# Optimization experiments

Hardware: AMD Instinct MI355X
Metric: run time of the kernel (lower is better)

## Reference

```python
import jax, jax.numpy as jnp
import numpy as np

HEADS = 16
DIM_HEAD = 64
RMS_EPS = 1.1920929e-07  # torch.finfo(float32).eps (torch RMSNorm eps=None default)
ROPE_THETA = 10000.0


def _rope(x):
    # x: [b, h, n, d]; rotary-embedding-torch style interleaved rotation
    n, d = x.shape[-2], x.shape[-1]
    inv_freq = 1.0 / (ROPE_THETA ** (jnp.arange(0, d, 2, dtype=jnp.float32) / d))
    t = jnp.arange(n, dtype=jnp.float32)
    freqs = t[:, None] * inv_freq[None, :]              # [n, d/2]
    cos = jnp.repeat(jnp.cos(freqs), 2, axis=-1)        # [n, d] interleaved
    sin = jnp.repeat(jnp.sin(freqs), 2, axis=-1)
    x1 = x[..., ::2]
    x2 = x[..., 1::2]
    rot = jnp.stack((-x2, x1), axis=-1).reshape(x.shape)  # rotate_half, interleaved pairs
    return x * cos + rot * sin


def setup_inputs() -> dict:
    key = jax.random.key(0)
    ks = jax.random.split(key, 6)
    b, n, dim = 2, 2048, 1024
    tokens = jax.random.normal(ks[0], (b, n, dim), dtype=jnp.float32)
    norm_weight = jnp.ones((dim,), dtype=jnp.float32)
    wq = jax.random.normal(ks[1], (dim, dim), dtype=jnp.float32) * 0.02
    wk = jax.random.normal(ks[2], (dim, dim), dtype=jnp.float32) * 0.02
    wv = jax.random.normal(ks[3], (dim, dim), dtype=jnp.float32) * 0.02
    wo = jax.random.normal(ks[4], (dim, dim), dtype=jnp.float32) * 0.02
    return {"tokens": tokens, "norm_weight": norm_weight, "wq": wq, "wk": wk, "wv": wv, "wo": wo}


def reference(tokens, norm_weight, wq, wk, wv, wo):
    b, n, dim = tokens.shape
    # RMSNorm (elementwise affine)
    x = tokens * jax.lax.rsqrt(jnp.mean(tokens * tokens, axis=-1, keepdims=True) + RMS_EPS)
    x = x * norm_weight
    # QKV projections (torch Linear: x @ W.T), split heads: b n (h d) -> b h n d
    def split(y):
        return y.reshape(b, n, HEADS, DIM_HEAD).transpose(0, 2, 1, 3)
    q = split(x @ wq.T) * (DIM_HEAD ** -0.5)
    k = split(x @ wk.T)
    v = split(x @ wv.T)
    # rotary embedding (no kv cache -> same positions for q and k)
    q = _rope(q)
    k = _rope(k)
    sim = jnp.einsum('bhid,bhjd->bhij', q, k)
    causal = jnp.triu(jnp.ones((n, n), dtype=bool), k=1)
    sim = jnp.where(causal, -jnp.finfo(sim.dtype).max, sim)
    attn = jax.nn.softmax(sim, axis=-1)
    out = jnp.einsum('bhij,bhjd->bhid', attn, v)
    out = out.transpose(0, 2, 1, 3).reshape(b, n, dim)  # merge heads
    return out @ wo.T
```

## Files before the change

kernel.cpp:

```cpp
#include <hip/hip_runtime.h>

typedef __bf16 bf16x8 __attribute__((ext_vector_type(8)));
typedef float f32x4 __attribute__((ext_vector_type(4)));

#define DIM 1024
#define NSEQ 2048

#define GL2LDS(g, l) __builtin_amdgcn_global_load_lds( \
    (const __attribute__((address_space(1))) void*)(g), \
    (__attribute__((address_space(3))) void*)(l), 16, 0, 0)

__global__ __launch_bounds__(256) void cvt_kernel(const float* __restrict__ s,
                                                  __bf16* __restrict__ d) {
    int i = (blockIdx.x * 256 + threadIdx.x) * 4;
    float4 f = *(const float4*)(s + i);
    union { uint2 u; __bf16 h[4]; } p;
    p.h[0] = (__bf16)f.x; p.h[1] = (__bf16)f.y;
    p.h[2] = (__bf16)f.z; p.h[3] = (__bf16)f.w;
    *(uint2*)(d + i) = p.u;
}

__global__ __launch_bounds__(256) void cvt3_kernel(const float* __restrict__ wq,
                                                   const float* __restrict__ wk,
                                                   const float* __restrict__ wv,
                                                   __bf16* __restrict__ dq,
                                                   __bf16* __restrict__ dk,
                                                   __bf16* __restrict__ dv,
                                                   int* __restrict__ counters) {
    if (blockIdx.x == 0 && blockIdx.y == 0 && threadIdx.x < 8)
        counters[threadIdx.x] = 0;
    const float* s = blockIdx.y == 0 ? wq : (blockIdx.y == 1 ? wk : wv);
    __bf16*      d = blockIdx.y == 0 ? dq : (blockIdx.y == 1 ? dk : dv);
    int i = (blockIdx.x * 256 + threadIdx.x) * 4;
    float4 f = *(const float4*)(s + i);
    union { uint2 u; __bf16 h[4]; } p;
    p.h[0] = (__bf16)f.x; p.h[1] = (__bf16)f.y;
    p.h[2] = (__bf16)f.z; p.h[3] = (__bf16)f.w;
    *(uint2*)(d + i) = p.u;
}

__global__ __launch_bounds__(256) void rmsnorm_kernel(const float* __restrict__ x,
                                                      const float* __restrict__ g,
                                                      __bf16* __restrict__ o) {
    int row = blockIdx.x;
    int t = threadIdx.x;
    float4 xv = ((const float4*)(x + (size_t)row * DIM))[t];
    float ss = xv.x*xv.x + xv.y*xv.y + xv.z*xv.z + xv.w*xv.w;
    #pragma unroll
    for (int off = 32; off; off >>= 1) ss += __shfl_xor(ss, off, 64);
    __shared__ float red[4];
    if ((t & 63) == 0) red[t >> 6] = ss;
    __syncthreads();
    ss = red[0] + red[1] + red[2] + red[3];
    float r = rsqrtf(ss * (1.0f / 1024.0f) + 1.1920929e-07f);
    float4 gv = ((const float4*)g)[t];
    union { uint2 u; __bf16 h[4]; } p;
    p.h[0] = (__bf16)(xv.x * r * gv.x);
    p.h[1] = (__bf16)(xv.y * r * gv.y);
    p.h[2] = (__bf16)(xv.z * r * gv.z);
    p.h[3] = (__bf16)(xv.w * r * gv.w);
    *(uint2*)(o + (size_t)row * DIM + t * 4) = p.u;
}

__global__ __launch_bounds__(256) void rope_kernel(__bf16* __restrict__ qb,
                                                   __bf16* __restrict__ kb) {
    int bid = blockIdx.x;
    __bf16* x = (bid & 1) ? kb : qb;
    int gid = (bid >> 1) * 256 + threadIdx.x;
    int row = gid >> 9;
    int pr = gid & 511;
    int pos = row & (NSEQ - 1);
    int dp = pr & 31;
    float inv = __expf(-(float)dp * (9.210340371976184f / 32.0f));
    float ang = (float)pos * inv;
    float sn, cs;
    sincosf(ang, &sn, &cs);
    size_t off = (size_t)row * DIM + pr * 2;
    union { unsigned int u; __bf16 h[2]; } p;
    p.u = *(const unsigned int*)(x + off);
    float x1 = (float)p.h[0], x2 = (float)p.h[1];
    p.h[0] = (__bf16)(x1 * cs - x2 * sn);
    p.h[1] = (__bf16)(x2 * cs + x1 * sn);
    *(unsigned int*)(x + off) = p.u;
}

template <typename CT>
__device__ __forceinline__ void gemm_body(const __bf16* __restrict__ A,
                                          const __bf16* __restrict__ B,
                                          CT* __restrict__ C,
                                          int mb, int nb, int ldc, float scale,
                                          __bf16* As, __bf16* Bs) {
    int t = threadIdx.x;
    int w = t >> 6, l = t & 63;
    int wm = (w >> 1) * 64, wn = (w & 1) * 64;
    int lrow = l & 15, lq = l >> 4;
    f32x4 acc[4][4] = {};

    int srow = w * 32 + (l >> 3);
    int sc8 = (l & 7) * 8;
    const __bf16* gA = A + (size_t)(mb * 128 + srow) * 1024 + sc8;
    const __bf16* gB = B + (size_t)(nb * 128 + srow) * 1024 + sc8;
    __bf16* lA = As + (size_t)(w * 32) * 64;
    __bf16* lB = Bs + (size_t)(w * 32) * 64;

    for (int kt = 0; kt < 16; ++kt) {
        int k0 = kt * 64;
        #pragma unroll
        for (int c = 0; c < 4; ++c) {
            GL2LDS(gA + (size_t)c * 8 * 1024 + k0, lA + c * 8 * 64);
            GL2LDS(gB + (size_t)c * 8 * 1024 + k0, lB + c * 8 * 64);
        }
        __syncthreads();
        #pragma unroll
        for (int ch = 0; ch < 2; ++ch) {
            bf16x8 af[4], bfr[4];
            #pragma unroll
            for (int i = 0; i < 4; ++i)
                af[i] = *(const bf16x8*)&As[(wm + i * 16 + lrow) * 64 + ch * 32 + lq * 8];
            #pragma unroll
            for (int i = 0; i < 4; ++i)
                bfr[i] = *(const bf16x8*)&Bs[(wn + i * 16 + lrow) * 64 + ch * 32 + lq * 8];
            #pragma unroll
            for (int rt = 0; rt < 4; ++rt)
                #pragma unroll
                for (int ct = 0; ct < 4; ++ct)
                    acc[rt][ct] = __builtin_amdgcn_mfma_f32_16x16x32_bf16(
                        af[rt], bfr[ct], acc[rt][ct], 0, 0, 0);
        }
        __syncthreads();
    }
    #pragma unroll
    for (int rt = 0; rt < 4; ++rt)
        #pragma unroll
        for (int ct = 0; ct < 4; ++ct)
            #pragma unroll
            for (int r = 0; r < 4; ++r) {
                int row = mb * 128 + wm + rt * 16 + lq * 4 + r;
                int col = nb * 128 + wn + ct * 16 + lrow;
                C[(size_t)row * ldc + col] = (CT)(acc[rt][ct][r] * scale);
            }
}

__global__ __launch_bounds__(256) void qkv_kernel(const __bf16* __restrict__ x,
                                                  const __bf16* __restrict__ wq,
                                                  const __bf16* __restrict__ wk,
                                                  const __bf16* __restrict__ wv,
                                                  __bf16* __restrict__ qb,
                                                  __bf16* __restrict__ kb,
                                                  __bf16* __restrict__ vtb) {
    __shared__ __bf16 As[128 * 64];
    __shared__ __bf16 Bs[128 * 64];
    int bm = blockIdx.x, bn = blockIdx.y, z = blockIdx.z;
    if (z == 0)      gemm_body<__bf16>(x,  wq, qb,  bm, bn, 1024,
                                       0.125f * 1.44269504088896340736f, As, Bs);
    else if (z == 1) gemm_body<__bf16>(x,  wk, kb,  bm, bn, 1024, 1.0f,   As, Bs);
    else             gemm_body<__bf16>(wv, x,  vtb, bn, bm, 4096, 1.0f,   As, Bs);
}

__global__ __launch_bounds__(256) void wo_kernel(const __bf16* __restrict__ A,
                                                 const __bf16* __restrict__ B,
                                                 float* __restrict__ C) {
    __shared__ __bf16 As[128 * 64];
    __shared__ __bf16 Bs[128 * 64];
    gemm_body<float>(A, B, C, blockIdx.x, blockIdx.y, 1024, 1.0f, As, Bs);
}

__global__ __launch_bounds__(256, 3) void attn_kernel(const __bf16* __restrict__ q,
                                                      const __bf16* __restrict__ kk,
                                                      const __bf16* __restrict__ vt,
                                                      __bf16* __restrict__ o,
                                                      int* __restrict__ counters) {
    int xcd = blockIdx.x & 7;
    int t = threadIdx.x;
    int w = t >> 6, l = t & 63;
    int lrow = l & 15, lq = l >> 4;
    int row0 = t >> 3;
    int c8 = (t & 7) * 8;

    __shared__ __bf16 Kt[2][64 * 72];
    __shared__ __bf16 Vs[2][64 * 72];
    __shared__ __bf16 Ps[4 * 16 * 72];
    __shared__ int s_item;
    __bf16* pw = &Ps[w * 16 * 72];

    for (;;) {
        if (t == 0) s_item = atomicAdd(&counters[xcd], 1);
        __syncthreads();
        int item = s_item;
        if (item >= 128) break;
        int qt = 31 - (item >> 2);
        int bh = xcd * 4 + (item & 3);
        int h = bh & 15;
        int b = bh >> 4;
        int rowbase = b * NSEQ;

        const __bf16* kbase = kk + (size_t)rowbase * DIM + h * 64;
        const __bf16* vbase = vt + (size_t)(h * 64) * 4096 + b * 2048;

        const __bf16* qp = q + (size_t)(rowbase + qt * 64 + w * 16 + lrow) * DIM + h * 64;
        bf16x8 qb0 = *(const bf16x8*)(qp + lq * 8);
        bf16x8 qb1 = *(const bf16x8*)(qp + 32 + lq * 8);

        f32x4 oacc[4] = {};
        float m_r = -1e30f, l_r = 0.0f;

        uint4 kr0, kr1, vr0, vr1;
        kr0 = *(const uint4*)(kbase + (size_t)row0 * DIM + c8);
        kr1 = *(const uint4*)(kbase + (size_t)(row0 + 32) * DIM + c8);
        vr0 = *(const uint4*)(vbase + (size_t)row0 * 4096 + c8);
        vr1 = *(const uint4*)(vbase + (size_t)(row0 + 32) * 4096 + c8);
        *(uint4*)&Kt[0][row0 * 72 + c8] = kr0;
        *(uint4*)&Kt[0][(row0 + 32) * 72 + c8] = kr1;
        *(uint4*)&Vs[0][row0 * 72 + c8] = vr0;
        *(uint4*)&Vs[0][(row0 + 32) * 72 + c8] = vr1;
        __syncthreads();

        for (int jt = 0; jt <= qt; ++jt) {
            int cur = jt & 1;
            if (jt < qt) {
                int j0 = (jt + 1) * 64;
                kr0 = *(const uint4*)(kbase + (size_t)(j0 + row0) * DIM + c8);
                kr1 = *(const uint4*)(kbase + (size_t)(j0 + row0 + 32) * DIM + c8);
                vr0 = *(const uint4*)(vbase + (size_t)row0 * 4096 + j0 + c8);
                vr1 = *(const uint4*)(vbase + (size_t)(row0 + 32) * 4096 + j0 + c8);
            }
            f32x4 st[4];
            #pragma unroll
            for (int ct = 0; ct < 4; ++ct) {
                f32x4 z = {};
                bf16x8 ka0 = *(const bf16x8*)&Kt[cur][(ct * 16 + lrow) * 72 + lq * 8];
                bf16x8 ka1 = *(const bf16x8*)&Kt[cur][(ct * 16 + lrow) * 72 + 32 + lq * 8];
                z = __builtin_amdgcn_mfma_f32_16x16x32_bf16(ka0, qb0, z, 0, 0, 0);
                z = __builtin_amdgcn_mfma_f32_16x16x32_bf16(ka1, qb1, z, 0, 0, 0);
                st[ct] = z;
            }
            if (jt == qt) {
                int qr = w * 16 + lrow;
                #pragma unroll
                for (int ct = 0; ct < 4; ++ct)
                    #pragma unroll
                    for (int r = 0; r < 4; ++r)
                        if (ct * 16 + lq * 4 + r > qr) st[ct][r] = -3.0e38f;
            }
            float mx = st[0][0];
            #pragma unroll
            for (int ct = 0; ct < 4; ++ct)
                #pragma unroll
                for (int r = 0; r < 4; ++r) mx = fmaxf(mx, st[ct][r]);
            mx = fmaxf(mx, __shfl_xor(mx, 16, 64));
            mx = fmaxf(mx, __shfl_xor(mx, 32, 64));
            if (!__all(mx - m_r <= 8.0f)) {
                float mnew = fmaxf(m_r, mx);
                float alpha = __builtin_amdgcn_exp2f(m_r - mnew);
                l_r *= alpha;
                #pragma unroll
                for (int ct = 0; ct < 4; ++ct)
                    #pragma unroll
                    for (int r = 0; r < 4; ++r) oacc[ct][r] *= alpha;
                m_r = mnew;
            }
            float ps = 0.0f;
            #pragma unroll
            for (int ct = 0; ct < 4; ++ct)
                #pragma unroll
                for (int r = 0; r < 4; ++r) {
                    float p = __builtin_amdgcn_exp2f(st[ct][r] - m_r);
                    st[ct][r] = p;
                    ps += p;
                }
            ps += __shfl_xor(ps, 16, 64);
            ps += __shfl_xor(ps, 32, 64);
            l_r += ps;

            #pragma unroll
            for (int ct = 0; ct < 4; ++ct) {
                union { uint2 u; __bf16 h4[4]; } pk;
                #pragma unroll
                for (int r = 0; r < 4; ++r) pk.h4[r] = (__bf16)st[ct][r];
                *(uint2*)&pw[lrow * 72 + ct * 16 + lq * 4] = pk.u;
            }
            bf16x8 pb0 = *(const bf16x8*)&pw[lrow * 72 + lq * 8];
            bf16x8 pb1 = *(const bf16x8*)&pw[lrow * 72 + 32 + lq * 8];
            #pragma unroll
            for (int ct = 0; ct < 4; ++ct) {
                bf16x8 va0 = *(const bf16x8*)&Vs[cur][(ct * 16 + lrow) * 72 + lq * 8];
                bf16x8 va1 = *(const bf16x8*)&Vs[cur][(ct * 16 + lrow) * 72 + 32 + lq * 8];
                oacc[ct] = __builtin_amdgcn_mfma_f32_16x16x32_bf16(va0, pb0, oacc[ct], 0, 0, 0);
                oacc[ct] = __builtin_amdgcn_mfma_f32_16x16x32_bf16(va1, pb1, oacc[ct], 0, 0, 0);
            }
            if (jt < qt) {
                *(uint4*)&Kt[cur ^ 1][row0 * 72 + c8] = kr0;
                *(uint4*)&Kt[cur ^ 1][(row0 + 32) * 72 + c8] = kr1;
                *(uint4*)&Vs[cur ^ 1][row0 * 72 + c8] = vr0;
                *(uint4*)&Vs[cur ^ 1][(row0 + 32) * 72 + c8] = vr1;
            }
            __syncthreads();
        }
        float rcp = 1.0f / l_r;
        const size_t orow = (size_t)(rowbase + qt * 64 + w * 16 + lrow) * DIM + h * 64;
        #pragma unroll
        for (int ct = 0; ct < 4; ++ct) {
            union { uint2 u; __bf16 h4[4]; } pk;
            #pragma unroll
            for (int r = 0; r < 4; ++r) pk.h4[r] = (__bf16)(oacc[ct][r] * rcp);
            *(uint2*)(o + orow + ct * 16 + lq * 4) = pk.u;
        }
    }
}

extern "C" void kernel_launch(void* const* d_in, const int* in_sizes, int n_in,
                              void* d_out, int out_size, void* d_ws, size_t ws_size,
                              hipStream_t stream) {
    const float* tokens = (const float*)d_in[0];
    const float* gamma  = (const float*)d_in[1];
    const float* wq = (const float*)d_in[2];
    const float* wk = (const float*)d_in[3];
    const float* wv = (const float*)d_in[4];
    const float* wo = (const float*)d_in[5];

    __bf16* ws  = (__bf16*)d_ws;
    __bf16* x   = ws;
    __bf16* qb  = x   + (size_t)4096 * 1024;
    __bf16* kb  = qb  + (size_t)4096 * 1024;
    __bf16* vtb = kb  + (size_t)4096 * 1024;
    __bf16* ao  = x;
    __bf16* wob = qb;
    float*  out = (float*)d_out;

    __bf16* wqb = (__bf16*)d_out;
    __bf16* wkb = wqb + (size_t)1024 * 1024;
    __bf16* wvb = wkb + (size_t)1024 * 1024;
    int* counters = (int*)((char*)d_out + (size_t)8 * 1024 * 1024);

    cvt3_kernel<<<dim3(1024, 3), 256, 0, stream>>>(wq, wk, wv, wqb, wkb, wvb, counters);

    rmsnorm_kernel<<<4096, 256, 0, stream>>>(tokens, gamma, x);

    qkv_kernel<<<dim3(32, 8, 3), 256, 0, stream>>>(x, wqb, wkb, wvb, qb, kb, vtb);

    rope_kernel<<<16384, 256, 0, stream>>>(qb, kb);

    attn_kernel<<<768, 256, 0, stream>>>(qb, kb, vtb, ao, counters);

    cvt_kernel<<<1024, 256, 0, stream>>>(wo, wob);

    wo_kernel<<<dim3(32, 8), 256, 0, stream>>>(ao, wob, out);
}
```

Measured before the change: 206.2 us.

## Software-pipeline QK^T one tile ahead of softmax in causal flash attention

Restructures the attention inner loop so the QK^T MFMAs for the next key tile are issued before the softmax of the current tile. Scores ping-pong between two register sets, global prefetch runs two tiles ahead, and s_setprio raises wave priority around the MFMA blocks. The max and sum reductions are also rewritten as trees to shorten dependency chains. In exchange it uses more registers, which may lower occupancy, and adds an extra barrier per iteration around the LDS buffer writes.

```diff
diff --git a/kernel.cpp b/kernel.cpp
--- a/kernel.cpp
+++ b/kernel.cpp
@@ -203,8 +203,9 @@
 
         f32x4 oacc[4] = {};
         float m_r = -1e30f, l_r = 0.0f;
-
+        f32x4 stA[4], stB[4];
         uint4 kr0, kr1, vr0, vr1;
+
         kr0 = *(const uint4*)(kbase + (size_t)row0 * DIM + c8);
         kr1 = *(const uint4*)(kbase + (size_t)(row0 + 32) * DIM + c8);
         vr0 = *(const uint4*)(vbase + (size_t)row0 * 4096 + c8);
@@ -213,26 +214,55 @@
         *(uint4*)&Kt[0][(row0 + 32) * 72 + c8] = kr1;
         *(uint4*)&Vs[0][row0 * 72 + c8] = vr0;
         *(uint4*)&Vs[0][(row0 + 32) * 72 + c8] = vr1;
+        if (qt >= 1) {
+            kr0 = *(const uint4*)(kbase + (size_t)(64 + row0) * DIM + c8);
+            kr1 = *(const uint4*)(kbase + (size_t)(64 + row0 + 32) * DIM + c8);
+            vr0 = *(const uint4*)(vbase + (size_t)row0 * 4096 + 64 + c8);
+            vr1 = *(const uint4*)(vbase + (size_t)(row0 + 32) * 4096 + 64 + c8);
+        }
         __syncthreads();
-
-        for (int jt = 0; jt <= qt; ++jt) {
-            int cur = jt & 1;
-            if (jt < qt) {
-                int j0 = (jt + 1) * 64;
+        __builtin_amdgcn_s_setprio(1);
+        #pragma unroll
+        for (int ct = 0; ct < 4; ++ct) {
+            f32x4 z = {};
+            bf16x8 ka0 = *(const bf16x8*)&Kt[0][(ct * 16 + lrow) * 72 + lq * 8];
+            bf16x8 ka1 = *(const bf16x8*)&Kt[0][(ct * 16 + lrow) * 72 + 32 + lq * 8];
+            z = __builtin_amdgcn_mfma_f32_16x16x32_bf16(ka0, qb0, z, 0, 0, 0);
+            z = __builtin_amdgcn_mfma_f32_16x16x32_bf16(ka1, qb1, z, 0, 0, 0);
+            stA[ct] = z;
+        }
+        __builtin_amdgcn_s_setprio(0);
+        if (qt >= 1) {
+            *(uint4*)&Kt[1][row0 * 72 + c8] = kr0;
+            *(uint4*)&Kt[1][(row0 + 32) * 72 + c8] = kr1;
+            *(uint4*)&Vs[1][row0 * 72 + c8] = vr0;
+            *(uint4*)&Vs[1][(row0 + 32) * 72 + c8] = vr1;
+            __syncthreads();
+        }
+
+        auto trip = [&](f32x4 (&sc)[4], f32x4 (&sn)[4], int jt) {
+            bool nx1 = jt + 1 <= qt;
+            bool nx2 = jt + 2 <= qt;
+            if (nx2) {
+                int j0 = (jt + 2) * 64;
                 kr0 = *(const uint4*)(kbase + (size_t)(j0 + row0) * DIM + c8);
                 kr1 = *(const uint4*)(kbase + (size_t)(j0 + row0 + 32) * DIM + c8);
                 vr0 = *(const uint4*)(vbase + (size_t)row0 * 4096 + j0 + c8);
                 vr1 = *(const uint4*)(vbase + (size_t)(row0 + 32) * 4096 + j0 + c8);
             }
-            f32x4 st[4];
-            #pragma unroll
-            for (int ct = 0; ct < 4; ++ct) {
-                f32x4 z = {};
-                bf16x8 ka0 = *(const bf16x8*)&Kt[cur][(ct * 16 + lrow) * 72 + lq * 8];
-                bf16x8 ka1 = *(const bf16x8*)&Kt[cur][(ct * 16 + lrow) * 72 + 32 + lq * 8];
-                z = __builtin_amdgcn_mfma_f32_16x16x32_bf16(ka0, qb0, z, 0, 0, 0);
-                z = __builtin_amdgcn_mfma_f32_16x16x32_bf16(ka1, qb1, z, 0, 0, 0);
-                st[ct] = z;
+            if (nx1) {
+                int kc = (jt + 1) & 1;
+                __builtin_amdgcn_s_setprio(1);
+                #pragma unroll
+                for (int ct = 0; ct < 4; ++ct) {
+                    f32x4 z = {};
+                    bf16x8 ka0 = *(const bf16x8*)&Kt[kc][(ct * 16 + lrow) * 72 + lq * 8];
+                    bf16x8 ka1 = *(const bf16x8*)&Kt[kc][(ct * 16 + lrow) * 72 + 32 + lq * 8];
+                    z = __builtin_amdgcn_mfma_f32_16x16x32_bf16(ka0, qb0, z, 0, 0, 0);
+                    z = __builtin_amdgcn_mfma_f32_16x16x32_bf16(ka1, qb1, z, 0, 0, 0);
+                    sn[ct] = z;
+                }
+                __builtin_amdgcn_s_setprio(0);
             }
             if (jt == qt) {
                 int qr = w * 16 + lrow;
@@ -240,13 +270,13 @@
                 for (int ct = 0; ct < 4; ++ct)
                     #pragma unroll
                     for (int r = 0; r < 4; ++r)
-                        if (ct * 16 + lq * 4 + r > qr) st[ct][r] = -3.0e38f;
-            }
-            float mx = st[0][0];
-            #pragma unroll
-            for (int ct = 0; ct < 4; ++ct)
-                #pragma unroll
-                for (int r = 0; r < 4; ++r) mx = fmaxf(mx, st[ct][r]);
+                        if (ct * 16 + lq * 4 + r > qr) sc[ct][r] = -3.0e38f;
+            }
+            float m0 = fmaxf(fmaxf(sc[0][0], sc[0][1]), fmaxf(sc[0][2], sc[0][3]));
+            float m1 = fmaxf(fmaxf(sc[1][0], sc[1][1]), fmaxf(sc[1][2], sc[1][3]));
+            float m2 = fmaxf(fmaxf(sc[2][0], sc[2][1]), fmaxf(sc[2][2], sc[2][3]));
+            float m3 = fmaxf(fmaxf(sc[3][0], sc[3][1]), fmaxf(sc[3][2], sc[3][3]));
+            float mx = fmaxf(fmaxf(m0, m1), fmaxf(m2, m3));
             mx = fmaxf(mx, __shfl_xor(mx, 16, 64));
             mx = fmaxf(mx, __shfl_xor(mx, 32, 64));
             if (!__all(mx - m_r <= 8.0f)) {
@@ -259,15 +289,19 @@
                     for (int r = 0; r < 4; ++r) oacc[ct][r] *= alpha;
                 m_r = mnew;
             }
-            float ps = 0.0f;
-            #pragma unroll
-            for (int ct = 0; ct < 4; ++ct)
+            float psum[4];
+            #pragma unroll
+            for (int ct = 0; ct < 4; ++ct) {
+                float s = 0.0f;
                 #pragma unroll
                 for (int r = 0; r < 4; ++r) {
-                    float p = __builtin_amdgcn_exp2f(st[ct][r] - m_r);
-                    st[ct][r] = p;
-                    ps += p;
+                    float p = __builtin_amdgcn_exp2f(sc[ct][r] - m_r);
+                    sc[ct][r] = p;
+                    s += p;
                 }
+                psum[ct] = s;
+            }
+            float ps = (psum[0] + psum[1]) + (psum[2] + psum[3]);
             ps += __shfl_xor(ps, 16, 64);
             ps += __shfl_xor(ps, 32, 64);
             l_r += ps;
@@ -276,26 +310,42 @@
             for (int ct = 0; ct < 4; ++ct) {
                 union { uint2 u; __bf16 h4[4]; } pk;
                 #pragma unroll
-                for (int r = 0; r < 4; ++r) pk.h4[r] = (__bf16)st[ct][r];
+                for (int r = 0; r < 4; ++r) pk.h4[r] = (__bf16)sc[ct][r];
                 *(uint2*)&pw[lrow * 72 + ct * 16 + lq * 4] = pk.u;
             }
             bf16x8 pb0 = *(const bf16x8*)&pw[lrow * 72 + lq * 8];
             bf16x8 pb1 = *(const bf16x8*)&pw[lrow * 72 + 32 + lq * 8];
+            int vc = jt & 1;
+            __builtin_amdgcn_s_setprio(1);
             #pragma unroll
             for (int ct = 0; ct < 4; ++ct) {
-                bf16x8 va0 = *(const bf16x8*)&Vs[cur][(ct * 16 + lrow) * 72 + lq * 8];
-                bf16x8 va1 = *(const bf16x8*)&Vs[cur][(ct * 16 + lrow) * 72 + 32 + lq * 8];
+                bf16x8 va0 = *(const bf16x8*)&Vs[vc][(ct * 16 + lrow) * 72 + lq * 8];
+                bf16x8 va1 = *(const bf16x8*)&Vs[vc][(ct * 16 + lrow) * 72 + 32 + lq * 8];
                 oacc[ct] = __builtin_amdgcn_mfma_f32_16x16x32_bf16(va0, pb0, oacc[ct], 0, 0, 0);
                 oacc[ct] = __builtin_amdgcn_mfma_f32_16x16x32_bf16(va1, pb1, oacc[ct], 0, 0, 0);
             }
-            if (jt < qt) {
-                *(uint4*)&Kt[cur ^ 1][row0 * 72 + c8] = kr0;
-                *(uint4*)&Kt[cur ^ 1][(row0 + 32) * 72 + c8] = kr1;
-                *(uint4*)&Vs[cur ^ 1][row0 * 72 + c8] = vr0;
-                *(uint4*)&Vs[cur ^ 1][(row0 + 32) * 72 + c8] = vr1;
-            }
-            __syncthreads();
-        }
+            __builtin_amdgcn_s_setprio(0);
+            if (nx2) {
+                __syncthreads();
+                int sb = jt & 1;
+                *(uint4*)&Kt[sb][row0 * 72 + c8] = kr0;
+                *(uint4*)&Kt[sb][(row0 + 32) * 72 + c8] = kr1;
+                *(uint4*)&Vs[sb][row0 * 72 + c8] = vr0;
+                *(uint4*)&Vs[sb][(row0 + 32) * 72 + c8] = vr1;
+                __syncthreads();
+            }
+        };
+
+        int jt = 0;
+        for (;;) {
+            trip(stA, stB, jt);
+            if (jt == qt) break;
+            ++jt;
+            trip(stB, stA, jt);
+            if (jt == qt) break;
+            ++jt;
+        }
+
         float rcp = 1.0f / l_r;
         const size_t orow = (size_t)(rowbase + qt * 64 + w * 16 + lrow) * DIM + h * 64;
         #pragma unroll
```

After: 204.4 us. About the same (-0.8%).

## Make attention waves independent with register-resident K/V and per-wave work stealing

Applied to the files above, without the earlier changes.

The attention kernel no longer stages K and V tiles through shared memory with block-wide barriers. Each wave now claims its own 32-row query tile from the per-XCD atomic counter and loads K/V fragments straight from global memory into registers, double-buffered through a two-step unrolled loop. The grid shrinks to 256 blocks and the occupancy hint is dropped. This removes the __syncthreads and LDS round-trips and improves causal load balance. In exchange, each wave re-reads K/V from L2 separately, which raises global traffic, and register pressure goes up.

```diff
diff --git a/kernel.cpp b/kernel.cpp
--- a/kernel.cpp
+++ b/kernel.cpp
@@ -9,6 +9,8 @@
 #define GL2LDS(g, l) __builtin_amdgcn_global_load_lds( \
     (const __attribute__((address_space(1))) void*)(g), \
     (__attribute__((address_space(3))) void*)(l), 16, 0, 0)
+
+#define MFMA16(a, b, c) __builtin_amdgcn_mfma_f32_16x16x32_bf16(a, b, c, 0, 0, 0)
 
 __global__ __launch_bounds__(256) void cvt_kernel(const float* __restrict__ s,
                                                   __bf16* __restrict__ d) {
@@ -124,8 +126,7 @@
             for (int rt = 0; rt < 4; ++rt)
                 #pragma unroll
                 for (int ct = 0; ct < 4; ++ct)
-                    acc[rt][ct] = __builtin_amdgcn_mfma_f32_16x16x32_bf16(
-                        af[rt], bfr[ct], acc[rt][ct], 0, 0, 0);
+                    acc[rt][ct] = MFMA16(af[rt], bfr[ct], acc[rt][ct]);
         }
         __syncthreads();
     }
@@ -165,145 +166,169 @@
     gemm_body<float>(A, B, C, blockIdx.x, blockIdx.y, 1024, 1.0f, As, Bs);
 }
 
-__global__ __launch_bounds__(256, 3) void attn_kernel(const __bf16* __restrict__ q,
-                                                      const __bf16* __restrict__ kk,
-                                                      const __bf16* __restrict__ vt,
-                                                      __bf16* __restrict__ o,
-                                                      int* __restrict__ counters) {
+__global__ __launch_bounds__(256) void attn_kernel(const __bf16* __restrict__ q,
+                                                   const __bf16* __restrict__ kk,
+                                                   const __bf16* __restrict__ vt,
+                                                   __bf16* __restrict__ o,
+                                                   int* __restrict__ counters) {
     int xcd = blockIdx.x & 7;
     int t = threadIdx.x;
     int w = t >> 6, l = t & 63;
     int lrow = l & 15, lq = l >> 4;
-    int row0 = t >> 3;
-    int c8 = (t & 7) * 8;
-
-    __shared__ __bf16 Kt[2][64 * 72];
-    __shared__ __bf16 Vs[2][64 * 72];
-    __shared__ __bf16 Ps[4 * 16 * 72];
-    __shared__ int s_item;
-    __bf16* pw = &Ps[w * 16 * 72];
+
+    __shared__ __bf16 Ps[4][32 * 76];
+    __bf16* pw = Ps[w];
 
     for (;;) {
-        if (t == 0) s_item = atomicAdd(&counters[xcd], 1);
-        __syncthreads();
-        int item = s_item;
-        if (item >= 128) break;
-        int qt = 31 - (item >> 2);
-        int bh = xcd * 4 + (item & 3);
+        int it = 0;
+        if (l == 0) it = atomicAdd(&counters[xcd], 1);
+        it = __shfl(it, 0, 64);
+        if (it >= 256) break;
+        int qq = 63 - (it >> 2);
+        int bh = xcd * 4 + (it & 3);
         int h = bh & 15;
         int b = bh >> 4;
         int rowbase = b * NSEQ;
+        int JT = qq >> 1;
 
         const __bf16* kbase = kk + (size_t)rowbase * DIM + h * 64;
         const __bf16* vbase = vt + (size_t)(h * 64) * 4096 + b * 2048;
 
-        const __bf16* qp = q + (size_t)(rowbase + qt * 64 + w * 16 + lrow) * DIM + h * 64;
-        bf16x8 qb0 = *(const bf16x8*)(qp + lq * 8);
-        bf16x8 qb1 = *(const bf16x8*)(qp + 32 + lq * 8);
-
-        f32x4 oacc[4] = {};
-        float m_r = -1e30f, l_r = 0.0f;
-
-        uint4 kr0, kr1, vr0, vr1;
-        kr0 = *(const uint4*)(kbase + (size_t)row0 * DIM + c8);
-        kr1 = *(const uint4*)(kbase + (size_t)(row0 + 32) * DIM + c8);
-        vr0 = *(const uint4*)(vbase + (size_t)row0 * 4096 + c8);
-        vr1 = *(const uint4*)(vbase + (size_t)(row0 + 32) * 4096 + c8);
-        *(uint4*)&Kt[0][row0 * 72 + c8] = kr0;
-        *(uint4*)&Kt[0][(row0 + 32) * 72 + c8] = kr1;
-        *(uint4*)&Vs[0][row0 * 72 + c8] = vr0;
-        *(uint4*)&Vs[0][(row0 + 32) * 72 + c8] = vr1;
-        __syncthreads();
-
-        for (int jt = 0; jt <= qt; ++jt) {
-            int cur = jt & 1;
-            if (jt < qt) {
-                int j0 = (jt + 1) * 64;
-                kr0 = *(const uint4*)(kbase + (size_t)(j0 + row0) * DIM + c8);
-                kr1 = *(const uint4*)(kbase + (size_t)(j0 + row0 + 32) * DIM + c8);
-                vr0 = *(const uint4*)(vbase + (size_t)row0 * 4096 + j0 + c8);
-                vr1 = *(const uint4*)(vbase + (size_t)(row0 + 32) * 4096 + j0 + c8);
-            }
-            f32x4 st[4];
-            #pragma unroll
-            for (int ct = 0; ct < 4; ++ct) {
-                f32x4 z = {};
-                bf16x8 ka0 = *(const bf16x8*)&Kt[cur][(ct * 16 + lrow) * 72 + lq * 8];
-                bf16x8 ka1 = *(const bf16x8*)&Kt[cur][(ct * 16 + lrow) * 72 + 32 + lq * 8];
-                z = __builtin_amdgcn_mfma_f32_16x16x32_bf16(ka0, qb0, z, 0, 0, 0);
-                z = __builtin_amdgcn_mfma_f32_16x16x32_bf16(ka1, qb1, z, 0, 0, 0);
-                st[ct] = z;
-            }
-            if (jt == qt) {
-                int qr = w * 16 + lrow;
+        bf16x8 qf[2][2];
+        #pragma unroll
+        for (int g = 0; g < 2; ++g) {
+            const __bf16* qp = q + (size_t)(rowbase + qq * 32 + g * 16 + lrow) * DIM + h * 64;
+            qf[g][0] = *(const bf16x8*)(qp + lq * 8);
+            qf[g][1] = *(const bf16x8*)(qp + 32 + lq * 8);
+        }
+
+        f32x4 oacc[2][4] = {};
+        float m_r[2] = {-1e30f, -1e30f};
+        float l_r[2] = {0.0f, 0.0f};
+
+        bf16x8 kA[8], kB[8], vA[8], vB[8];
+        #pragma unroll
+        for (int ct = 0; ct < 4; ++ct) {
+            const __bf16* kp = kbase + (size_t)(ct * 16 + lrow) * DIM;
+            kA[ct * 2]     = *(const bf16x8*)(kp + lq * 8);
+            kA[ct * 2 + 1] = *(const bf16x8*)(kp + 32 + lq * 8);
+            const __bf16* vp = vbase + (size_t)(ct * 16 + lrow) * 4096;
+            vA[ct * 2]     = *(const bf16x8*)(vp + lq * 8);
+            vA[ct * 2 + 1] = *(const bf16x8*)(vp + 32 + lq * 8);
+        }
+
+        auto trip = [&](bf16x8 (&kc)[8], bf16x8 (&kn)[8],
+                        bf16x8 (&vc)[8], bf16x8 (&vn)[8], int jt) {
+            f32x4 st[2][4];
+            #pragma unroll
+            for (int ct = 0; ct < 4; ++ct)
+                #pragma unroll
+                for (int g = 0; g < 2; ++g) {
+                    f32x4 z = {};
+                    z = MFMA16(kc[ct * 2],     qf[g][0], z);
+                    z = MFMA16(kc[ct * 2 + 1], qf[g][1], z);
+                    st[g][ct] = z;
+                }
+            if (jt < JT) {
+                int j1 = (jt + 1) * 64;
+                #pragma unroll
+                for (int ct = 0; ct < 4; ++ct) {
+                    const __bf16* kp = kbase + (size_t)(j1 + ct * 16 + lrow) * DIM;
+                    kn[ct * 2]     = *(const bf16x8*)(kp + lq * 8);
+                    kn[ct * 2 + 1] = *(const bf16x8*)(kp + 32 + lq * 8);
+                    const __bf16* vp = vbase + (size_t)(ct * 16 + lrow) * 4096 + j1;
+                    vn[ct * 2]     = *(const bf16x8*)(vp + lq * 8);
+                    vn[ct * 2 + 1] = *(const bf16x8*)(vp + 32 + lq * 8);
+                }
+            }
+            if (jt == JT) {
+                #pragma unroll
+                for (int g = 0; g < 2; ++g) {
+                    int qr = qq * 32 + g * 16 + lrow - JT * 64;
+                    #pragma unroll
+                    for (int ct = 0; ct < 4; ++ct)
+                        #pragma unroll
+                        for (int r = 0; r < 4; ++r)
+                            if (ct * 16 + lq * 4 + r > qr) st[g][ct][r] = -3.0e38f;
+                }
+            }
+            #pragma unroll
+            for (int g = 0; g < 2; ++g) {
+                float m0 = fmaxf(fmaxf(st[g][0][0], st[g][0][1]), fmaxf(st[g][0][2], st[g][0][3]));
+                float m1 = fmaxf(fmaxf(st[g][1][0], st[g][1][1]), fmaxf(st[g][1][2], st[g][1][3]));
+                float m2 = fmaxf(fmaxf(st[g][2][0], st[g][2][1]), fmaxf(st[g][2][2], st[g][2][3]));
+                float m3 = fmaxf(fmaxf(st[g][3][0], st[g][3][1]), fmaxf(st[g][3][2], st[g][3][3]));
+                float mx = fmaxf(fmaxf(m0, m1), fmaxf(m2, m3));
+                mx = fmaxf(mx, __shfl_xor(mx, 16, 64));
+                mx = fmaxf(mx, __shfl_xor(mx, 32, 64));
+                if (!__all(mx - m_r[g] <= 8.0f)) {
+                    float mnew = fmaxf(m_r[g], mx);
+                    float alpha = __builtin_amdgcn_exp2f(m_r[g] - mnew);
+                    l_r[g] *= alpha;
+                    #pragma unroll
+                    for (int ct = 0; ct < 4; ++ct)
+                        #pragma unroll
+                        for (int r = 0; r < 4; ++r) oacc[g][ct][r] *= alpha;
+                    m_r[g] = mnew;
+                }
+                float ps = 0.0f;
                 #pragma unroll
                 for (int ct = 0; ct < 4; ++ct)
                     #pragma unroll
-                    for (int r = 0; r < 4; ++r)
-                        if (ct * 16 + lq * 4 + r > qr) st[ct][r] = -3.0e38f;
-            }
-            float mx = st[0][0];
+                    for (int r = 0; r < 4; ++r) {
+                        float p = __builtin_amdgcn_exp2f(st[g][ct][r] - m_r[g]);
+                        st[g][ct][r] = p;
+                        ps += p;
+                    }
+                ps += __shfl_xor(ps, 16, 64);
+                ps += __shfl_xor(ps, 32, 64);
+                l_r[g] += ps;
+            }
+            #pragma unroll
+            for (int g = 0; g < 2; ++g)
+                #pragma unroll
+                for (int ct = 0; ct < 4; ++ct) {
+                    union { uint2 u; __bf16 h4[4]; } pk;
+                    #pragma unroll
+                    for (int r = 0; r < 4; ++r) pk.h4[r] = (__bf16)st[g][ct][r];
+                    *(uint2*)&pw[(g * 16 + lrow) * 76 + ct * 16 + lq * 4] = pk.u;
+                }
+            bf16x8 pb[2][2];
+            #pragma unroll
+            for (int g = 0; g < 2; ++g) {
+                pb[g][0] = *(const bf16x8*)&pw[(g * 16 + lrow) * 76 + lq * 8];
+                pb[g][1] = *(const bf16x8*)&pw[(g * 16 + lrow) * 76 + 32 + lq * 8];
+            }
             #pragma unroll
             for (int ct = 0; ct < 4; ++ct)
                 #pragma unroll
-                for (int r = 0; r < 4; ++r) mx = fmaxf(mx, st[ct][r]);
-            mx = fmaxf(mx, __shfl_xor(mx, 16, 64));
-            mx = fmaxf(mx, __shfl_xor(mx, 32, 64));
-            if (!__all(mx - m_r <= 8.0f)) {
-                float mnew = fmaxf(m_r, mx);
-                float alpha = __builtin_amdgcn_exp2f(m_r - mnew);
-                l_r *= alpha;
-                #pragma unroll
-                for (int ct = 0; ct < 4; ++ct)
-                    #pragma unroll
-                    for (int r = 0; r < 4; ++r) oacc[ct][r] *= alpha;
-                m_r = mnew;
-            }
-            float ps = 0.0f;
-            #pragma unroll
-            for (int ct = 0; ct < 4; ++ct)
-                #pragma unroll
-                for (int r = 0; r < 4; ++r) {
-                    float p = __builtin_amdgcn_exp2f(st[ct][r] - m_r);
-                    st[ct][r] = p;
-                    ps += p;
-                }
-            ps += __shfl_xor(ps, 16, 64);
-            ps += __shfl_xor(ps, 32, 64);
-            l_r += ps;
-
+                for (int g = 0; g < 2; ++g) {
+                    oacc[g][ct] = MFMA16(vc[ct * 2],     pb[g][0], oacc[g][ct]);
+                    oacc[g][ct] = MFMA16(vc[ct * 2 + 1], pb[g][1], oacc[g][ct]);
+                }
+        };
+
+        int jt = 0;
+        for (;;) {
+            trip(kA, kB, vA, vB, jt);
+            if (jt == JT) break;
+            ++jt;
+            trip(kB, kA, vB, vA, jt);
+            if (jt == JT) break;
+            ++jt;
+        }
+
+        #pragma unroll
+        for (int g = 0; g < 2; ++g) {
+            float rcp = 1.0f / l_r[g];
+            const size_t orow = (size_t)(rowbase + qq * 32 + g * 16 + lrow) * DIM + h * 64;
             #pragma unroll
             for (int ct = 0; ct < 4; ++ct) {
                 union { uint2 u; __bf16 h4[4]; } pk;
                 #pragma unroll
-                for (int r = 0; r < 4; ++r) pk.h4[r] = (__bf16)st[ct][r];
-                *(uint2*)&pw[lrow * 72 + ct * 16 + lq * 4] = pk.u;
-            }
-            bf16x8 pb0 = *(const bf16x8*)&pw[lrow * 72 + lq * 8];
-            bf16x8 pb1 = *(const bf16x8*)&pw[lrow * 72 + 32 + lq * 8];
-            #pragma unroll
-            for (int ct = 0; ct < 4; ++ct) {
-                bf16x8 va0 = *(const bf16x8*)&Vs[cur][(ct * 16 + lrow) * 72 + lq * 8];
-                bf16x8 va1 = *(const bf16x8*)&Vs[cur][(ct * 16 + lrow) * 72 + 32 + lq * 8];
-                oacc[ct] = __builtin_amdgcn_mfma_f32_16x16x32_bf16(va0, pb0, oacc[ct], 0, 0, 0);
-                oacc[ct] = __builtin_amdgcn_mfma_f32_16x16x32_bf16(va1, pb1, oacc[ct], 0, 0, 0);
-            }
-            if (jt < qt) {
-                *(uint4*)&Kt[cur ^ 1][row0 * 72 + c8] = kr0;
-                *(uint4*)&Kt[cur ^ 1][(row0 + 32) * 72 + c8] = kr1;
-                *(uint4*)&Vs[cur ^ 1][row0 * 72 + c8] = vr0;
-                *(uint4*)&Vs[cur ^ 1][(row0 + 32) * 72 + c8] = vr1;
-            }
-            __syncthreads();
-        }
-        float rcp = 1.0f / l_r;
-        const size_t orow = (size_t)(rowbase + qt * 64 + w * 16 + lrow) * DIM + h * 64;
-        #pragma unroll
-        for (int ct = 0; ct < 4; ++ct) {
-            union { uint2 u; __bf16 h4[4]; } pk;
-            #pragma unroll
-            for (int r = 0; r < 4; ++r) pk.h4[r] = (__bf16)(oacc[ct][r] * rcp);
-            *(uint2*)(o + orow + ct * 16 + lq * 4) = pk.u;
+                for (int r = 0; r < 4; ++r) pk.h4[r] = (__bf16)(oacc[g][ct][r] * rcp);
+                *(uint2*)(o + orow + ct * 16 + lq * 4) = pk.u;
+            }
         }
     }
 }
@@ -340,7 +365,7 @@
 
     rope_kernel<<<16384, 256, 0, stream>>>(qb, kb);
 
-    attn_kernel<<<768, 256, 0, stream>>>(qb, kb, vtb, ao, counters);
+    attn_kernel<<<256, 256, 0, stream>>>(qb, kb, vtb, ao, counters);
 
     cvt_kernel<<<1024, 256, 0, stream>>>(wo, wob);
 
```

Result: slower. 239.0 us (+15.9%).
